# Optimization experiments

Hardware: AMD Instinct MI355X
Metric: run time of the kernel (lower is better)

## Reference

```python
import jax, jax.numpy as jnp
import numpy as np

N_NODES = 100000
N_EDGES = 1600000
N_GRAPHS = 128
IN_FEATS = 128
OUT_FEATS = 64


def setup_inputs() -> dict:
    key = jax.random.key(0)
    k1, k2, k3, k4, k5, k6 = jax.random.split(key, 6)
    features = jax.random.normal(k1, (N_NODES, IN_FEATS), jnp.float32)
    src = jax.random.randint(k2, (N_EDGES,), 0, N_NODES, dtype=jnp.int32)
    dst = jax.random.randint(k3, (N_EDGES,), 0, N_NODES, dtype=jnp.int32)
    graph_ids = jnp.sort(jax.random.randint(k4, (N_NODES,), 0, N_GRAPHS, dtype=jnp.int32))
    # Xavier-uniform init as in DGL GraphConv
    lim1 = float(np.sqrt(6.0 / (IN_FEATS + IN_FEATS)))
    lim2 = float(np.sqrt(6.0 / (IN_FEATS + OUT_FEATS)))
    W1 = jax.random.uniform(k5, (IN_FEATS, IN_FEATS), jnp.float32, -lim1, lim1)
    W2 = jax.random.uniform(k6, (IN_FEATS, OUT_FEATS), jnp.float32, -lim2, lim2)
    b1 = jnp.zeros((IN_FEATS,), jnp.float32)
    b2 = jnp.zeros((OUT_FEATS,), jnp.float32)
    return {"features": features, "W1": W1, "b1": b1, "W2": W2, "b2": b2,
            "src": src, "dst": dst, "graph_ids": graph_ids, "num_graphs": N_GRAPHS}


def _graph_conv(x, W, b, src, dst, n_nodes):
    # DGL GraphConv, norm='both': D_dst^{-1/2} A D_src^{-1/2} X W + b
    ones = jnp.ones(src.shape, x.dtype)
    deg_out = jax.ops.segment_sum(ones, src, num_segments=n_nodes)
    deg_in = jax.ops.segment_sum(ones, dst, num_segments=n_nodes)
    norm_src = jax.lax.rsqrt(jnp.maximum(deg_out, 1.0))  # [N]
    norm_dst = jax.lax.rsqrt(jnp.maximum(deg_in, 1.0))   # [N]
    h = (x * norm_src[:, None]) @ W                       # dense transform first
    agg = jax.ops.segment_sum(h[src], dst, num_segments=n_nodes)  # spmm-style scatter-add
    return agg * norm_dst[:, None] + b


def reference(features, W1, b1, W2, b2, src, dst, graph_ids, num_graphs):
    n = features.shape[0]
    h = jax.nn.relu(_graph_conv(features, W1, b1, src, dst, n))
    h = jax.nn.relu(_graph_conv(h, W2, b2, src, dst, n))
    # dgl.mean_nodes: per-graph mean over nodes
    sums = jax.ops.segment_sum(h, graph_ids, num_segments=num_graphs)
    counts = jax.ops.segment_sum(jnp.ones((n, 1), h.dtype), graph_ids, num_segments=num_graphs)
    return sums / jnp.maximum(counts, 1.0)
```

## Files before the change

### kernel.cpp

```cpp
#include <hip/hip_runtime.h>
#include <hip/hip_bf16.h>


#define NPP_SHIFT 9
#define NPP 512
#define MAXP 256
#define NB 512

typedef __attribute__((ext_vector_type(8))) short frag8;
typedef __attribute__((ext_vector_type(4))) float f32x4;

__launch_bounds__(256)
__global__ void passA_count(const int* __restrict__ src, const int* __restrict__ dst,
                            int E, int P, int* __restrict__ counts_src,
                            int* __restrict__ counts_dst) {
    __shared__ int h1[MAXP], h2[MAXP];
    int tid = threadIdx.x;
    for (int i = tid; i < P; i += 256) { h1[i] = 0; h2[i] = 0; }
    __syncthreads();
    int per_block = (E + NB - 1) / NB;
    int e0 = blockIdx.x * per_block;
    int e1 = min(e0 + per_block, E);
    for (int e = e0 + tid; e < e1; e += 256) {
        atomicAdd(&h1[src[e] >> NPP_SHIFT], 1);
        atomicAdd(&h2[dst[e] >> NPP_SHIFT], 1);
    }
    __syncthreads();
    for (int i = tid; i < P; i += 256) {
        counts_src[(size_t)blockIdx.x * P + i] = h1[i];
        counts_dst[(size_t)blockIdx.x * P + i] = h2[i];
    }
}

__launch_bounds__(1024)
__global__ void scanB(const int* __restrict__ counts, int* __restrict__ offs,
                      int* __restrict__ ptot, int P) {
    __shared__ int s[1024];
    int tid = threadIdx.x;
    int p = blockIdx.x % P;
    int st = blockIdx.x / P;
    const int* c = counts + (size_t)st * NB * P;
    int v = (tid < NB) ? c[(size_t)tid * P + p] : 0;
    s[tid] = v;
    __syncthreads();
    for (int off = 1; off < 1024; off <<= 1) {
        int t = (tid >= off) ? s[tid - off] : 0;
        __syncthreads();
        s[tid] += t;
        __syncthreads();
    }
    if (tid < NB) offs[(size_t)st * NB * P + (size_t)tid * P + p] = s[tid] - v;
    if (tid == 1023) ptot[st * P + p] = s[1023];
}

__launch_bounds__(256)
__global__ void passC_scatter(const int* __restrict__ src, const int* __restrict__ dst,
                              int E, int P, const int* __restrict__ offs,
                              const int* __restrict__ ptot, int* __restrict__ pbase,
                              int* __restrict__ ebuf_src, int2* __restrict__ ebuf_dst) {
    __shared__ int cur1[MAXP], cur2[MAXP], sc[256];
    int tid = threadIdx.x;
    int v = (tid < P) ? ptot[tid] : 0;
    sc[tid] = v;
    __syncthreads();
    for (int off = 1; off < 256; off <<= 1) {
        int t = (tid >= off) ? sc[tid - off] : 0;
        __syncthreads();
        sc[tid] += t;
        __syncthreads();
    }
    int base0 = sc[tid] - v;
    if (tid < P) {
        cur1[tid] = base0 + offs[(size_t)blockIdx.x * P + tid];
        if (blockIdx.x == 0) pbase[tid] = base0;
    }
    __syncthreads();
    v = (tid < P) ? ptot[P + tid] : 0;
    sc[tid] = v;
    __syncthreads();
    for (int off = 1; off < 256; off <<= 1) {
        int t = (tid >= off) ? sc[tid - off] : 0;
        __syncthreads();
        sc[tid] += t;
        __syncthreads();
    }
    int base1 = sc[tid] - v;
    if (tid < P) {
        cur2[tid] = base1 + offs[(size_t)NB * P + (size_t)blockIdx.x * P + tid];
        if (blockIdx.x == 0) pbase[P + tid] = base1;
    }
    __syncthreads();
    int per_block = (E + NB - 1) / NB;
    int e0 = blockIdx.x * per_block;
    int e1 = min(e0 + per_block, E);
    for (int e = e0 + tid; e < e1; e += 256) {
        int s = src[e];
        int d = dst[e];
        int pos1 = atomicAdd(&cur1[s >> NPP_SHIFT], 1);
        ebuf_src[pos1] = s;
        int pos2 = atomicAdd(&cur2[d >> NPP_SHIFT], 1);
        ebuf_dst[pos2] = make_int2(d, s);
    }
}

__launch_bounds__(512)
__global__ void passD_build(const int* __restrict__ ebuf_src, const int2* __restrict__ ebuf_dst,
                            const int* __restrict__ ptot, const int* __restrict__ pbase,
                            float* __restrict__ norm_src, int* __restrict__ row_start,
                            int* __restrict__ csr_src, int N, int E, int P) {
    __shared__ int hs[NPP], hd[NPP], sc[NPP];
    int tid = threadIdx.x;
    int p = blockIdx.x;
    int node_lo = p << NPP_SHIFT;
    int nl = min(NPP, N - node_lo);
    hs[tid] = 0;
    hd[tid] = 0;
    __syncthreads();
    int nsrc = ptot[p];
    int base_s = pbase[p];
    for (int i = tid; i < nsrc; i += 512)
        atomicAdd(&hs[ebuf_src[base_s + i] - node_lo], 1);
    int ndst = ptot[P + p];
    int base_d = pbase[P + p];
    for (int i = tid; i < ndst; i += 512)
        atomicAdd(&hd[ebuf_dst[base_d + i].x - node_lo], 1);
    __syncthreads();
    if (tid < nl) norm_src[node_lo + tid] = rsqrtf((float)max(hs[tid], 1));
    int myh = hd[tid];
    sc[tid] = myh;
    __syncthreads();
    for (int off = 1; off < 512; off <<= 1) {
        int t = (tid >= off) ? sc[tid - off] : 0;
        __syncthreads();
        sc[tid] += t;
        __syncthreads();
    }
    int row0 = base_d + sc[tid] - myh;
    if (tid < nl) row_start[node_lo + tid] = row0;
    if (p == P - 1 && tid == 0) row_start[N] = E;
    __syncthreads();
    hd[tid] = row0;
    __syncthreads();
    for (int i = tid; i < ndst; i += 512) {
        int2 r = ebuf_dst[base_d + i];
        int pos = atomicAdd(&hd[r.x - node_lo], 1);
        csr_src[pos] = r.y;
    }
}

template <int COLS, bool BF16IN>
__launch_bounds__(256)
__global__ void gemm_mfma(const void* __restrict__ xin, const float* __restrict__ w,
                          const float* __restrict__ norm,
                          __hip_bfloat16* __restrict__ out, int n) {
    constexpr int NT = COLS / 16;
    __shared__ short wlds[4 * NT * 64 * 8];
    const int tid = threadIdx.x;
    for (int i = tid; i < 128 * COLS / 4; i += 256) {
        int k = (i * 4) / COLS;
        int n0 = (i * 4) % COLS;
        float4 wv = reinterpret_cast<const float4*>(w)[i];
        int c = k >> 5, q = (k >> 3) & 3, j = k & 7;
        float vals[4] = {wv.x, wv.y, wv.z, wv.w};
#pragma unroll
        for (int u = 0; u < 4; ++u) {
            int nn = n0 + u;
            int t = nn >> 4;
            int ln = (q << 4) | (nn & 15);
            union { __hip_bfloat16 b; short s; } cv;
            cv.b = __float2bfloat16(vals[u]);
            wlds[(((c * NT + t) << 6) | ln) * 8 + j] = cv.s;
        }
    }
    __syncthreads();

    const int lane = tid & 63;
    const int wid = tid >> 6;
    const int m = lane & 15;
    const int q = lane >> 4;
    const int ntiles = (n + 15) >> 4;
    const frag8* wfr = reinterpret_cast<const frag8*>(wlds);

    for (int wt = blockIdx.x * 4 + wid; wt < ntiles; wt += gridDim.x * 4) {
        const int row = (wt << 4) + m;
        frag8 af[4];
        if (row < n) {
            if constexpr (BF16IN) {
                const frag8* xp = reinterpret_cast<const frag8*>(
                    (const __hip_bfloat16*)xin + (size_t)row * 128);
#pragma unroll
                for (int c = 0; c < 4; ++c) af[c] = xp[c * 4 + q];
            } else {
                const float* xp = (const float*)xin + (size_t)row * 128;
                float nm = norm[row];
#pragma unroll
                for (int c = 0; c < 4; ++c) {
                    int base = c * 32 + q * 8;
                    float4 v0 = *reinterpret_cast<const float4*>(xp + base);
                    float4 v1 = *reinterpret_cast<const float4*>(xp + base + 4);
                    union { frag8 f; short s[8]; } a;
                    union { __hip_bfloat16 b; short s; } cv;
                    cv.b = __float2bfloat16(v0.x * nm); a.s[0] = cv.s;
                    cv.b = __float2bfloat16(v0.y * nm); a.s[1] = cv.s;
                    cv.b = __float2bfloat16(v0.z * nm); a.s[2] = cv.s;
                    cv.b = __float2bfloat16(v0.w * nm); a.s[3] = cv.s;
                    cv.b = __float2bfloat16(v1.x * nm); a.s[4] = cv.s;
                    cv.b = __float2bfloat16(v1.y * nm); a.s[5] = cv.s;
                    cv.b = __float2bfloat16(v1.z * nm); a.s[6] = cv.s;
                    cv.b = __float2bfloat16(v1.w * nm); a.s[7] = cv.s;
                    af[c] = a.f;
                }
            }
        } else {
#pragma unroll
            for (int c = 0; c < 4; ++c) af[c] = frag8{0, 0, 0, 0, 0, 0, 0, 0};
        }
        f32x4 acc[NT] = {};
#pragma unroll
        for (int c = 0; c < 4; ++c)
#pragma unroll
            for (int t = 0; t < NT; ++t)
                acc[t] = __builtin_amdgcn_mfma_f32_16x16x32_bf16(
                    af[c], wfr[(c * NT + t) * 64 + lane], acc[t], 0, 0, 0);
#pragma unroll
        for (int r = 0; r < 4; ++r) {
            int grow = (wt << 4) + q * 4 + r;
            if (grow < n) {
#pragma unroll
                for (int t = 0; t < NT; ++t)
                    out[(size_t)grow * COLS + t * 16 + m] = __float2bfloat16(acc[t][r]);
            }
        }
    }
}

__launch_bounds__(256)
__global__ void spmm1_kernel(const __hip_bfloat16* __restrict__ h,
                             const int* __restrict__ row_start,
                             const int* __restrict__ csr_src,
                             const float* __restrict__ b1,
                             const float* __restrict__ norm_src,
                             uint* __restrict__ out, int n) {
    int gw = (blockIdx.x * blockDim.x + threadIdx.x) >> 6;
    int lane = threadIdx.x & 63;
    if (gw >= n) return;
    int e0 = row_start[gw];
    int e1 = row_start[gw + 1];
    const uint* hp = reinterpret_cast<const uint*>(h);
    float2 acc = {0.f, 0.f};
    int e = e0;
    for (; e + 16 <= e1; e += 16) {
        uint v[16];
#pragma unroll
        for (int j = 0; j < 16; ++j)
            v[j] = hp[(size_t)csr_src[e + j] * 64 + lane];
#pragma unroll
        for (int j = 0; j < 16; ++j) {
            acc.x += __uint_as_float(v[j] << 16);
            acc.y += __uint_as_float(v[j] & 0xffff0000u);
        }
    }
    if (e + 8 <= e1) {
        uint v[8];
#pragma unroll
        for (int j = 0; j < 8; ++j)
            v[j] = hp[(size_t)csr_src[e + j] * 64 + lane];
#pragma unroll
        for (int j = 0; j < 8; ++j) {
            acc.x += __uint_as_float(v[j] << 16);
            acc.y += __uint_as_float(v[j] & 0xffff0000u);
        }
        e += 8;
    }
    if (e + 4 <= e1) {
        uint v[4];
#pragma unroll
        for (int j = 0; j < 4; ++j)
            v[j] = hp[(size_t)csr_src[e + j] * 64 + lane];
#pragma unroll
        for (int j = 0; j < 4; ++j) {
            acc.x += __uint_as_float(v[j] << 16);
            acc.y += __uint_as_float(v[j] & 0xffff0000u);
        }
        e += 4;
    }
    if (e + 2 <= e1) {
        uint v0 = hp[(size_t)csr_src[e] * 64 + lane];
        uint v1 = hp[(size_t)csr_src[e + 1] * 64 + lane];
        acc.x += __uint_as_float(v0 << 16);
        acc.y += __uint_as_float(v0 & 0xffff0000u);
        acc.x += __uint_as_float(v1 << 16);
        acc.y += __uint_as_float(v1 & 0xffff0000u);
        e += 2;
    }
    if (e < e1) {
        uint v0 = hp[(size_t)csr_src[e] * 64 + lane];
        acc.x += __uint_as_float(v0 << 16);
        acc.y += __uint_as_float(v0 & 0xffff0000u);
    }
    float nd = rsqrtf((float)max(e1 - e0, 1));
    float ns = norm_src[gw];
    float2 bb = reinterpret_cast<const float2*>(b1)[lane];
    float ox = fmaxf(fmaf(acc.x, nd, bb.x), 0.f) * ns;
    float oy = fmaxf(fmaf(acc.y, nd, bb.y), 0.f) * ns;
    union { __hip_bfloat16 b; ushort s; } cx, cy;
    cx.b = __float2bfloat16(ox);
    cy.b = __float2bfloat16(oy);
    out[(size_t)gw * 64 + lane] = (uint)cx.s | ((uint)cy.s << 16);
}

__launch_bounds__(256)
__global__ void spmm2_kernel(const __hip_bfloat16* __restrict__ h,
                             const int* __restrict__ row_start,
                             const int* __restrict__ csr_src,
                             const float* __restrict__ b2, ushort* __restrict__ y, int n) {
    int gw = (blockIdx.x * blockDim.x + threadIdx.x) >> 6;
    int lane = threadIdx.x & 63;
    if (gw >= n) return;
    int e0 = row_start[gw];
    int e1 = row_start[gw + 1];
    const ushort* hp = reinterpret_cast<const ushort*>(h);
    float acc = 0.f;
    int e = e0;
    for (; e + 16 <= e1; e += 16) {
        uint v[16];
#pragma unroll
        for (int j = 0; j < 16; ++j)
            v[j] = hp[(size_t)csr_src[e + j] * 64 + lane];
#pragma unroll
        for (int j = 0; j < 16; ++j) acc += __uint_as_float(v[j] << 16);
    }
    if (e + 8 <= e1) {
        uint v[8];
#pragma unroll
        for (int j = 0; j < 8; ++j)
            v[j] = hp[(size_t)csr_src[e + j] * 64 + lane];
#pragma unroll
        for (int j = 0; j < 8; ++j) acc += __uint_as_float(v[j] << 16);
        e += 8;
    }
    if (e + 4 <= e1) {
        uint v[4];
#pragma unroll
        for (int j = 0; j < 4; ++j)
            v[j] = hp[(size_t)csr_src[e + j] * 64 + lane];
#pragma unroll
        for (int j = 0; j < 4; ++j) acc += __uint_as_float(v[j] << 16);
        e += 4;
    }
    if (e + 2 <= e1) {
        uint v0 = hp[(size_t)csr_src[e] * 64 + lane];
        uint v1 = hp[(size_t)csr_src[e + 1] * 64 + lane];
        acc += __uint_as_float(v0 << 16);
        acc += __uint_as_float(v1 << 16);
        e += 2;
    }
    if (e < e1) {
        uint v0 = hp[(size_t)csr_src[e] * 64 + lane];
        acc += __uint_as_float(v0 << 16);
    }
    float nd = rsqrtf((float)max(e1 - e0, 1));
    float val = fmaxf(fmaf(acc, nd, b2[lane]), 0.f);
    union { __hip_bfloat16 b; ushort s; } cv;
    cv.b = __float2bfloat16(val);
    y[(size_t)gw * 64 + lane] = cv.s;
}

__launch_bounds__(256)
__global__ void pool_kernel(const ushort* __restrict__ y, const int* __restrict__ gids,
                            float* __restrict__ out, int n) {
    int g = blockIdx.x;
    int lo = 0, hi = n;
    while (lo < hi) {
        int mid = (lo + hi) >> 1;
        if (gids[mid] < g) lo = mid + 1; else hi = mid;
    }
    int s = lo;
    hi = n;
    while (lo < hi) {
        int mid = (lo + hi) >> 1;
        if (gids[mid] < g + 1) lo = mid + 1; else hi = mid;
    }
    int e = lo;
    int lane = threadIdx.x & 63;
    int wave = threadIdx.x >> 6;
    float acc = 0.f;
    int i = s + wave;
    for (; i + 12 < e; i += 16) {
        uint u0 = y[(size_t)(i + 0) * 64 + lane];
        uint u1 = y[(size_t)(i + 4) * 64 + lane];
        uint u2 = y[(size_t)(i + 8) * 64 + lane];
        uint u3 = y[(size_t)(i + 12) * 64 + lane];
        acc += __uint_as_float(u0 << 16) + __uint_as_float(u1 << 16) +
               __uint_as_float(u2 << 16) + __uint_as_float(u3 << 16);
    }
    for (; i < e; i += 4)
        acc += __uint_as_float((uint)y[(size_t)i * 64 + lane] << 16);
    __shared__ float sbuf[4][64];
    sbuf[wave][lane] = acc;
    __syncthreads();
    if (wave == 0) {
        float v = sbuf[0][lane] + sbuf[1][lane] + sbuf[2][lane] + sbuf[3][lane];
        out[(size_t)g * 64 + lane] = v / fmaxf((float)(e - s), 1.f);
    }
}

extern "C" void kernel_launch(void* const* d_in, const int* in_sizes, int n_in,
                              void* d_out, int out_size, void* d_ws, size_t ws_size,
                              hipStream_t stream) {
    const float* features = (const float*)d_in[0];
    const float* W1 = (const float*)d_in[1];
    const float* b1 = (const float*)d_in[2];
    const float* W2 = (const float*)d_in[3];
    const float* b2 = (const float*)d_in[4];
    const int* src = (const int*)d_in[5];
    const int* dst = (const int*)d_in[6];
    const int* gids = (const int*)d_in[7];
    const int N = in_sizes[7];
    const int E = in_sizes[5];
    const int G = out_size / 64;
    float* out = (float*)d_out;
    const int P = (N + NPP - 1) >> NPP_SHIFT;

    char* ws = (char*)d_ws;
    size_t off = 0;
    auto alloc = [&](size_t bytes) -> void* {
        void* p = ws + off;
        off = (off + bytes + 255) & ~(size_t)255;
        return p;
    };
    int* counts = (int*)alloc((size_t)2 * NB * P * 4);
    int* offs = (int*)alloc((size_t)2 * NB * P * 4);
    int* ptot = (int*)alloc((size_t)2 * P * 4);
    int* pbase = (int*)alloc((size_t)2 * P * 4);
    int* ebuf_src = (int*)alloc((size_t)E * 4);
    int2* ebuf_dst = (int2*)alloc((size_t)E * 8);
    float* norm_src = (float*)alloc((size_t)N * 4);
    int* row_start = (int*)alloc((size_t)(N + 1) * 4);
    int* csr_src = (int*)alloc((size_t)E * 4);
    __hip_bfloat16* h1 = (__hip_bfloat16*)alloc((size_t)N * 128 * 2);
    __hip_bfloat16* x2n = (__hip_bfloat16*)alloc((size_t)N * 128 * 2);
    ushort* y = (ushort*)alloc((size_t)N * 64 * 2);
    __hip_bfloat16* h2 = h1;

    const int B = 256;
    passA_count<<<NB, 256, 0, stream>>>(src, dst, E, P, counts, counts + (size_t)NB * P);
    scanB<<<2 * P, 1024, 0, stream>>>(counts, offs, ptot, P);
    passC_scatter<<<NB, 256, 0, stream>>>(src, dst, E, P, offs, ptot, pbase,
                                          ebuf_src, ebuf_dst);
    passD_build<<<P, 512, 0, stream>>>(ebuf_src, ebuf_dst, ptot, pbase, norm_src, row_start,
                                       csr_src, N, E, P);

    gemm_mfma<128, false><<<768, 256, 0, stream>>>(features, W1, norm_src, h1, N);
    spmm1_kernel<<<(N * 64 + B - 1) / B, B, 0, stream>>>(h1, row_start, csr_src, b1, norm_src,
                                                         (uint*)x2n, N);
    gemm_mfma<64, true><<<768, 256, 0, stream>>>(x2n, W2, nullptr, h2, N);
    spmm2_kernel<<<(N * 64 + B - 1) / B, B, 0, stream>>>(h2, row_start, csr_src, b2, y, N);
    pool_kernel<<<G, 256, 0, stream>>>(y, gids, out, N);
}
```

Before: 331.6 us.

## Store layer-1 transform in FP8 and fuse mean pooling into second SpMM

The first GEMM now writes its output as packed FP8 instead of bf16, halving the bytes gathered per edge in the first aggregation. Each wave processes two edges at once, one per half-wave, and a permuted W2 load undoes the resulting column order. Per-graph node counts are computed in the count pass, and the second aggregation atomically adds pre-scaled results into the output, removing the separate pooling kernel and the intermediate y buffer. FP8 loses precision and the float atomics make the summation order nondeterministic.

```diff
diff --git a/kernel.cpp b/kernel.cpp
--- a/kernel.cpp
+++ b/kernel.cpp
@@ -9,14 +9,17 @@
 
 typedef __attribute__((ext_vector_type(8))) short frag8;
 typedef __attribute__((ext_vector_type(4))) float f32x4;
+typedef __attribute__((ext_vector_type(2))) float v2f;
 
 __launch_bounds__(256)
 __global__ void passA_count(const int* __restrict__ src, const int* __restrict__ dst,
                             int E, int P, int* __restrict__ counts_src,
-                            int* __restrict__ counts_dst) {
-    __shared__ int h1[MAXP], h2[MAXP];
+                            int* __restrict__ counts_dst,
+                            const int* __restrict__ gids, int N, int G,
+                            int* __restrict__ gcnt) {
+    __shared__ int h1[MAXP], h2[MAXP], h3[MAXP];
     int tid = threadIdx.x;
-    for (int i = tid; i < P; i += 256) { h1[i] = 0; h2[i] = 0; }
+    for (int i = tid; i < MAXP; i += 256) { h1[i] = 0; h2[i] = 0; h3[i] = 0; }
     __syncthreads();
     int per_block = (E + NB - 1) / NB;
     int e0 = blockIdx.x * per_block;
@@ -25,11 +28,17 @@
         atomicAdd(&h1[src[e] >> NPP_SHIFT], 1);
         atomicAdd(&h2[dst[e] >> NPP_SHIFT], 1);
     }
+    int npb = (N + NB - 1) / NB;
+    int n0 = blockIdx.x * npb;
+    int n1 = min(n0 + npb, N);
+    for (int i = n0 + tid; i < n1; i += 256) atomicAdd(&h3[gids[i]], 1);
     __syncthreads();
     for (int i = tid; i < P; i += 256) {
         counts_src[(size_t)blockIdx.x * P + i] = h1[i];
         counts_dst[(size_t)blockIdx.x * P + i] = h2[i];
     }
+    for (int i = tid; i < G; i += 256)
+        if (h3[i]) atomicAdd(&gcnt[i], h3[i]);
 }
 
 __launch_bounds__(1024)
@@ -148,18 +157,24 @@
     }
 }
 
-template <int COLS, bool BF16IN>
+template <int COLS, bool BF16IN, bool PERM, bool FP8OUT>
 __launch_bounds__(256)
 __global__ void gemm_mfma(const void* __restrict__ xin, const float* __restrict__ w,
                           const float* __restrict__ norm,
-                          __hip_bfloat16* __restrict__ out, int n) {
+                          void* __restrict__ out, int n) {
     constexpr int NT = COLS / 16;
     __shared__ short wlds[4 * NT * 64 * 8];
     const int tid = threadIdx.x;
     for (int i = tid; i < 128 * COLS / 4; i += 256) {
         int k = (i * 4) / COLS;
         int n0 = (i * 4) % COLS;
-        float4 wv = reinterpret_cast<const float4*>(w)[i];
+        float4 wv;
+        if constexpr (PERM) {
+            int ksrc = 64 * ((k >> 2) & 1) + 16 * (k & 3) + (k >> 3);
+            wv = *reinterpret_cast<const float4*>(w + (size_t)ksrc * COLS + n0);
+        } else {
+            wv = reinterpret_cast<const float4*>(w)[i];
+        }
         int c = k >> 5, q = (k >> 3) & 3, j = k & 7;
         float vals[4] = {wv.x, wv.y, wv.z, wv.w};
 #pragma unroll
@@ -226,182 +241,174 @@
         for (int r = 0; r < 4; ++r) {
             int grow = (wt << 4) + q * 4 + r;
             if (grow < n) {
-#pragma unroll
-                for (int t = 0; t < NT; ++t)
-                    out[(size_t)grow * COLS + t * 16 + m] = __float2bfloat16(acc[t][r]);
+                if constexpr (FP8OUT) {
+                    uint w0 = 0, w1 = 0;
+                    w0 = (uint)__builtin_amdgcn_cvt_pk_fp8_f32(acc[0][r], acc[1][r], (int)w0, false);
+                    w0 = (uint)__builtin_amdgcn_cvt_pk_fp8_f32(acc[2][r], acc[3][r], (int)w0, true);
+                    w1 = (uint)__builtin_amdgcn_cvt_pk_fp8_f32(acc[4][r], acc[5][r], (int)w1, false);
+                    w1 = (uint)__builtin_amdgcn_cvt_pk_fp8_f32(acc[6][r], acc[7][r], (int)w1, true);
+                    reinterpret_cast<uint2*>(out)[(size_t)grow * 16 + m] = make_uint2(w0, w1);
+                } else {
+                    __hip_bfloat16* ob = reinterpret_cast<__hip_bfloat16*>(out);
+#pragma unroll
+                    for (int t = 0; t < NT; ++t)
+                        ob[(size_t)grow * COLS + t * 16 + m] = __float2bfloat16(acc[t][r]);
+                }
             }
         }
     }
 }
 
 __launch_bounds__(256)
-__global__ void spmm1_kernel(const __hip_bfloat16* __restrict__ h,
+__global__ void spmm1_kernel(const uint* __restrict__ h1,
                              const int* __restrict__ row_start,
                              const int* __restrict__ csr_src,
                              const float* __restrict__ b1,
                              const float* __restrict__ norm_src,
-                             uint* __restrict__ out, int n) {
+                             uint2* __restrict__ x2n, int n) {
     int gw = (blockIdx.x * blockDim.x + threadIdx.x) >> 6;
     int lane = threadIdx.x & 63;
     if (gw >= n) return;
     int e0 = row_start[gw];
     int e1 = row_start[gw + 1];
-    const uint* hp = reinterpret_cast<const uint*>(h);
-    float2 acc = {0.f, 0.f};
+    int a = lane >> 5;
+    int s = lane & 31;
+    float acc0 = 0.f, acc1 = 0.f, acc2 = 0.f, acc3 = 0.f;
     int e = e0;
     for (; e + 16 <= e1; e += 16) {
-        uint v[16];
-#pragma unroll
-        for (int j = 0; j < 16; ++j)
-            v[j] = hp[(size_t)csr_src[e + j] * 64 + lane];
-#pragma unroll
-        for (int j = 0; j < 16; ++j) {
-            acc.x += __uint_as_float(v[j] << 16);
-            acc.y += __uint_as_float(v[j] & 0xffff0000u);
-        }
-    }
-    if (e + 8 <= e1) {
         uint v[8];
 #pragma unroll
-        for (int j = 0; j < 8; ++j)
-            v[j] = hp[(size_t)csr_src[e + j] * 64 + lane];
-#pragma unroll
         for (int j = 0; j < 8; ++j) {
-            acc.x += __uint_as_float(v[j] << 16);
-            acc.y += __uint_as_float(v[j] & 0xffff0000u);
-        }
-        e += 8;
-    }
-    if (e + 4 <= e1) {
-        uint v[4];
-#pragma unroll
-        for (int j = 0; j < 4; ++j)
-            v[j] = hp[(size_t)csr_src[e + j] * 64 + lane];
-#pragma unroll
-        for (int j = 0; j < 4; ++j) {
-            acc.x += __uint_as_float(v[j] << 16);
-            acc.y += __uint_as_float(v[j] & 0xffff0000u);
-        }
-        e += 4;
-    }
-    if (e + 2 <= e1) {
-        uint v0 = hp[(size_t)csr_src[e] * 64 + lane];
-        uint v1 = hp[(size_t)csr_src[e + 1] * 64 + lane];
-        acc.x += __uint_as_float(v0 << 16);
-        acc.y += __uint_as_float(v0 & 0xffff0000u);
-        acc.x += __uint_as_float(v1 << 16);
-        acc.y += __uint_as_float(v1 & 0xffff0000u);
-        e += 2;
+            int cs = csr_src[e + 2 * j + a];
+            v[j] = h1[(size_t)cs * 32 + s];
+        }
+#pragma unroll
+        for (int j = 0; j < 8; ++j) {
+            v2f lo = __builtin_amdgcn_cvt_pk_f32_fp8((int)v[j], false);
+            v2f hi = __builtin_amdgcn_cvt_pk_f32_fp8((int)v[j], true);
+            acc0 += lo[0]; acc1 += lo[1]; acc2 += hi[0]; acc3 += hi[1];
+        }
     }
     if (e < e1) {
-        uint v0 = hp[(size_t)csr_src[e] * 64 + lane];
-        acc.x += __uint_as_float(v0 << 16);
-        acc.y += __uint_as_float(v0 & 0xffff0000u);
-    }
-    float nd = rsqrtf((float)max(e1 - e0, 1));
-    float ns = norm_src[gw];
-    float2 bb = reinterpret_cast<const float2*>(b1)[lane];
-    float ox = fmaxf(fmaf(acc.x, nd, bb.x), 0.f) * ns;
-    float oy = fmaxf(fmaf(acc.y, nd, bb.y), 0.f) * ns;
-    union { __hip_bfloat16 b; ushort s; } cx, cy;
-    cx.b = __float2bfloat16(ox);
-    cy.b = __float2bfloat16(oy);
-    out[(size_t)gw * 64 + lane] = (uint)cx.s | ((uint)cy.s << 16);
+        uint v[8];
+#pragma unroll
+        for (int j = 0; j < 8; ++j) {
+            int idx = e + 2 * j + a;
+            int cidx = min(idx, e1 - 1);
+            int cs = csr_src[cidx];
+            uint vv = h1[(size_t)cs * 32 + s];
+            v[j] = (idx < e1) ? vv : 0u;
+        }
+#pragma unroll
+        for (int j = 0; j < 8; ++j) {
+            v2f lo = __builtin_amdgcn_cvt_pk_f32_fp8((int)v[j], false);
+            v2f hi = __builtin_amdgcn_cvt_pk_f32_fp8((int)v[j], true);
+            acc0 += lo[0]; acc1 += lo[1]; acc2 += hi[0]; acc3 += hi[1];
+        }
+    }
+    acc0 += __shfl_xor(acc0, 32);
+    acc1 += __shfl_xor(acc1, 32);
+    acc2 += __shfl_xor(acc2, 32);
+    acc3 += __shfl_xor(acc3, 32);
+    if (a == 0) {
+        float nd = rsqrtf((float)max(e1 - e0, 1));
+        float ns = norm_src[gw];
+        int m2 = s >> 1;
+        int a2 = (s & 1) << 6;
+        float f0 = fmaxf(fmaf(acc0, nd, b1[a2 + m2]), 0.f) * ns;
+        float f1 = fmaxf(fmaf(acc1, nd, b1[a2 + 16 + m2]), 0.f) * ns;
+        float f2 = fmaxf(fmaf(acc2, nd, b1[a2 + 32 + m2]), 0.f) * ns;
+        float f3 = fmaxf(fmaf(acc3, nd, b1[a2 + 48 + m2]), 0.f) * ns;
+        union { __hip_bfloat16 b; ushort u; } c0, c1, c2, c3;
+        c0.b = __float2bfloat16(f0);
+        c1.b = __float2bfloat16(f1);
+        c2.b = __float2bfloat16(f2);
+        c3.b = __float2bfloat16(f3);
+        uint w0 = (uint)c0.u | ((uint)c1.u << 16);
+        uint w1 = (uint)c2.u | ((uint)c3.u << 16);
+        x2n[(size_t)gw * 32 + s] = make_uint2(w0, w1);
+    }
 }
 
 __launch_bounds__(256)
 __global__ void spmm2_kernel(const __hip_bfloat16* __restrict__ h,
                              const int* __restrict__ row_start,
                              const int* __restrict__ csr_src,
-                             const float* __restrict__ b2, ushort* __restrict__ y, int n) {
+                             const float* __restrict__ b2,
+                             const int* __restrict__ gids,
+                             const int* __restrict__ gcnt,
+                             float* __restrict__ out, int n) {
     int gw = (blockIdx.x * blockDim.x + threadIdx.x) >> 6;
     int lane = threadIdx.x & 63;
-    if (gw >= n) return;
-    int e0 = row_start[gw];
-    int e1 = row_start[gw + 1];
+    int wave = threadIdx.x >> 6;
     const ushort* hp = reinterpret_cast<const ushort*>(h);
-    float acc = 0.f;
-    int e = e0;
-    for (; e + 16 <= e1; e += 16) {
-        uint v[16];
-#pragma unroll
-        for (int j = 0; j < 16; ++j)
-            v[j] = hp[(size_t)csr_src[e + j] * 64 + lane];
-#pragma unroll
-        for (int j = 0; j < 16; ++j) acc += __uint_as_float(v[j] << 16);
-    }
-    if (e + 8 <= e1) {
-        uint v[8];
-#pragma unroll
-        for (int j = 0; j < 8; ++j)
-            v[j] = hp[(size_t)csr_src[e + j] * 64 + lane];
-#pragma unroll
-        for (int j = 0; j < 8; ++j) acc += __uint_as_float(v[j] << 16);
-        e += 8;
-    }
-    if (e + 4 <= e1) {
-        uint v[4];
-#pragma unroll
-        for (int j = 0; j < 4; ++j)
-            v[j] = hp[(size_t)csr_src[e + j] * 64 + lane];
-#pragma unroll
-        for (int j = 0; j < 4; ++j) acc += __uint_as_float(v[j] << 16);
-        e += 4;
-    }
-    if (e + 2 <= e1) {
-        uint v0 = hp[(size_t)csr_src[e] * 64 + lane];
-        uint v1 = hp[(size_t)csr_src[e + 1] * 64 + lane];
-        acc += __uint_as_float(v0 << 16);
-        acc += __uint_as_float(v1 << 16);
-        e += 2;
-    }
-    if (e < e1) {
-        uint v0 = hp[(size_t)csr_src[e] * 64 + lane];
-        acc += __uint_as_float(v0 << 16);
-    }
-    float nd = rsqrtf((float)max(e1 - e0, 1));
-    float val = fmaxf(fmaf(acc, nd, b2[lane]), 0.f);
-    union { __hip_bfloat16 b; ushort s; } cv;
-    cv.b = __float2bfloat16(val);
-    y[(size_t)gw * 64 + lane] = cv.s;
-}
-
-__launch_bounds__(256)
-__global__ void pool_kernel(const ushort* __restrict__ y, const int* __restrict__ gids,
-                            float* __restrict__ out, int n) {
-    int g = blockIdx.x;
-    int lo = 0, hi = n;
-    while (lo < hi) {
-        int mid = (lo + hi) >> 1;
-        if (gids[mid] < g) lo = mid + 1; else hi = mid;
-    }
-    int s = lo;
-    hi = n;
-    while (lo < hi) {
-        int mid = (lo + hi) >> 1;
-        if (gids[mid] < g + 1) lo = mid + 1; else hi = mid;
-    }
-    int e = lo;
-    int lane = threadIdx.x & 63;
-    int wave = threadIdx.x >> 6;
-    float acc = 0.f;
-    int i = s + wave;
-    for (; i + 12 < e; i += 16) {
-        uint u0 = y[(size_t)(i + 0) * 64 + lane];
-        uint u1 = y[(size_t)(i + 4) * 64 + lane];
-        uint u2 = y[(size_t)(i + 8) * 64 + lane];
-        uint u3 = y[(size_t)(i + 12) * 64 + lane];
-        acc += __uint_as_float(u0 << 16) + __uint_as_float(u1 << 16) +
-               __uint_as_float(u2 << 16) + __uint_as_float(u3 << 16);
-    }
-    for (; i < e; i += 4)
-        acc += __uint_as_float((uint)y[(size_t)i * 64 + lane] << 16);
+    float val = 0.f;
+    int g;
+    if (gw < n) {
+        g = gids[gw];
+        int e0 = row_start[gw];
+        int e1 = row_start[gw + 1];
+        float acc = 0.f;
+        int e = e0;
+        for (; e + 16 <= e1; e += 16) {
+            uint v[16];
+#pragma unroll
+            for (int j = 0; j < 16; ++j)
+                v[j] = hp[(size_t)csr_src[e + j] * 64 + lane];
+#pragma unroll
+            for (int j = 0; j < 16; ++j) acc += __uint_as_float(v[j] << 16);
+        }
+        if (e + 8 <= e1) {
+            uint v[8];
+#pragma unroll
+            for (int j = 0; j < 8; ++j)
+                v[j] = hp[(size_t)csr_src[e + j] * 64 + lane];
+#pragma unroll
+            for (int j = 0; j < 8; ++j) acc += __uint_as_float(v[j] << 16);
+            e += 8;
+        }
+        if (e + 4 <= e1) {
+            uint v[4];
+#pragma unroll
+            for (int j = 0; j < 4; ++j)
+                v[j] = hp[(size_t)csr_src[e + j] * 64 + lane];
+#pragma unroll
+            for (int j = 0; j < 4; ++j) acc += __uint_as_float(v[j] << 16);
+            e += 4;
+        }
+        if (e + 2 <= e1) {
+            uint v0 = hp[(size_t)csr_src[e] * 64 + lane];
+            uint v1 = hp[(size_t)csr_src[e + 1] * 64 + lane];
+            acc += __uint_as_float(v0 << 16);
+            acc += __uint_as_float(v1 << 16);
+            e += 2;
+        }
+        if (e < e1) {
+            uint v0 = hp[(size_t)csr_src[e] * 64 + lane];
+            acc += __uint_as_float(v0 << 16);
+        }
+        float nd = rsqrtf((float)max(e1 - e0, 1));
+        val = fmaxf(fmaf(acc, nd, b2[lane]), 0.f);
+        val *= 1.f / (float)max(gcnt[g], 1);
+    } else {
+        g = gids[n - 1];
+    }
     __shared__ float sbuf[4][64];
-    sbuf[wave][lane] = acc;
+    __shared__ int sg[4];
+    sbuf[wave][lane] = val;
+    if (lane == 0) sg[wave] = g;
     __syncthreads();
     if (wave == 0) {
-        float v = sbuf[0][lane] + sbuf[1][lane] + sbuf[2][lane] + sbuf[3][lane];
-        out[(size_t)g * 64 + lane] = v / fmaxf((float)(e - s), 1.f);
+        int g0 = sg[0], g1 = sg[1], g2 = sg[2], g3 = sg[3];
+        if (g0 == g1 && g1 == g2 && g2 == g3) {
+            float ssum = sbuf[0][lane] + sbuf[1][lane] + sbuf[2][lane] + sbuf[3][lane];
+            atomicAdd(&out[(size_t)g0 * 64 + lane], ssum);
+        } else {
+            atomicAdd(&out[(size_t)g0 * 64 + lane], sbuf[0][lane]);
+            atomicAdd(&out[(size_t)g1 * 64 + lane], sbuf[1][lane]);
+            atomicAdd(&out[(size_t)g2 * 64 + lane], sbuf[2][lane]);
+            atomicAdd(&out[(size_t)g3 * 64 + lane], sbuf[3][lane]);
+        }
     }
 }
 
@@ -433,28 +440,34 @@
     int* offs = (int*)alloc((size_t)2 * NB * P * 4);
     int* ptot = (int*)alloc((size_t)2 * P * 4);
     int* pbase = (int*)alloc((size_t)2 * P * 4);
+    int* gcnt = (int*)alloc((size_t)G * 4);
     int* ebuf_src = (int*)alloc((size_t)E * 4);
     int2* ebuf_dst = (int2*)alloc((size_t)E * 8);
     float* norm_src = (float*)alloc((size_t)N * 4);
     int* row_start = (int*)alloc((size_t)(N + 1) * 4);
     int* csr_src = (int*)alloc((size_t)E * 4);
-    __hip_bfloat16* h1 = (__hip_bfloat16*)alloc((size_t)N * 128 * 2);
+    uint* h1 = (uint*)alloc((size_t)N * 128);
     __hip_bfloat16* x2n = (__hip_bfloat16*)alloc((size_t)N * 128 * 2);
-    ushort* y = (ushort*)alloc((size_t)N * 64 * 2);
-    __hip_bfloat16* h2 = h1;
+    __hip_bfloat16* h2 = (__hip_bfloat16*)h1;
+
+    hipMemsetAsync(out, 0, (size_t)out_size * sizeof(float), stream);
+    hipMemsetAsync(gcnt, 0, (size_t)G * 4, stream);
 
     const int B = 256;
-    passA_count<<<NB, 256, 0, stream>>>(src, dst, E, P, counts, counts + (size_t)NB * P);
+    passA_count<<<NB, 256, 0, stream>>>(src, dst, E, P, counts, counts + (size_t)NB * P,
+                                        gids, N, G, gcnt);
     scanB<<<2 * P, 1024, 0, stream>>>(counts, offs, ptot, P);
     passC_scatter<<<NB, 256, 0, stream>>>(src, dst, E, P, offs, ptot, pbase,
                                           ebuf_src, ebuf_dst);
     passD_build<<<P, 512, 0, stream>>>(ebuf_src, ebuf_dst, ptot, pbase, norm_src, row_start,
                                        csr_src, N, E, P);
 
-    gemm_mfma<128, false><<<768, 256, 0, stream>>>(features, W1, norm_src, h1, N);
+    gemm_mfma<128, false, false, true><<<768, 256, 0, stream>>>(features, W1, norm_src,
+                                                                (void*)h1, N);
     spmm1_kernel<<<(N * 64 + B - 1) / B, B, 0, stream>>>(h1, row_start, csr_src, b1, norm_src,
-                                                         (uint*)x2n, N);
-    gemm_mfma<64, true><<<768, 256, 0, stream>>>(x2n, W2, nullptr, h2, N);
-    spmm2_kernel<<<(N * 64 + B - 1) / B, B, 0, stream>>>(h2, row_start, csr_src, b2, y, N);
-    pool_kernel<<<G, 256, 0, stream>>>(y, gids, out, N);
-}
+                                                         (uint2*)x2n, N);
+    gemm_mfma<64, true, true, false><<<768, 256, 0, stream>>>(x2n, W2, nullptr,
+                                                              (void*)h2, N);
+    spmm2_kernel<<<(N * 64 + B - 1) / B, B, 0, stream>>>(h2, row_start, csr_src, b2,
+                                                         gids, gcnt, out, N);
+}
```

New measurement: 305.1 us. -8.0%, faster.
